# Optimization experiments

Measured on AMD Instinct MI355X. Metric: run time of the kernel, lower is better.

Reference implementation:

```python
import jax, jax.numpy as jnp
import numpy as np

NUM_HEADS = 16


def setup_inputs() -> dict:
    key = jax.random.key(0)
    ks = jax.random.split(key, 5)
    B, S, D = 2, 2048, 1024
    x = jax.random.normal(ks[0], (B, S, D), dtype=jnp.float32)
    # torch Linear weights are [out_features, in_features]; y = x @ W.T + b
    Wq = jax.random.normal(ks[1], (D, D), dtype=jnp.float32) * (D ** -0.5)
    Wk = jax.random.normal(ks[2], (D, D), dtype=jnp.float32) * (D ** -0.5)
    Wv = jax.random.normal(ks[3], (D, D), dtype=jnp.float32) * (D ** -0.5)
    Wo = jax.random.normal(ks[4], (D, D), dtype=jnp.float32) * (D ** -0.5)
    bo = jnp.zeros((D,), dtype=jnp.float32)
    return {"x": x, "Wq": Wq, "Wk": Wk, "Wv": Wv, "Wo": Wo, "bo": bo}


def reference(x, Wq, Wk, Wv, Wo, bo):
    B, S, D = x.shape
    H = NUM_HEADS
    dh = D // H
    # projections (torch Linear: x @ W.T)
    q = (x @ Wq.T).reshape(B, S, H, dh).transpose(0, 2, 1, 3)  # [B,H,S,dh]
    k = (x @ Wk.T).reshape(B, S, H, dh).transpose(0, 2, 1, 3)
    v = (x @ Wv.T).reshape(B, S, H, dh).transpose(0, 2, 1, 3)
    # NOTE: original code takes shape[-1] of the TRANSPOSED key (n,H,dh,S),
    # so the softmax scale is seq_length**-0.5 (a bug we reproduce faithfully).
    scale = jnp.asarray(S, x.dtype) ** -0.5
    scores = jnp.einsum("bhqd,bhkd->bhqk", q, k)  # [B,H,S,S]
    causal = jnp.triu(jnp.ones((S, S), dtype=bool), k=1)
    scores = jnp.where(causal, -jnp.inf, scores * scale)
    weights = jax.nn.softmax(scores, axis=-1)
    # dropout p=0.0 -> identity
    ctx = jnp.einsum("bhqk,bhkd->bhqd", weights, v)  # [B,H,S,dh]
    ctx = ctx.transpose(0, 2, 1, 3).reshape(B, S, D)
    return ctx @ Wo.T + bo
```

## Files before the change

kernel.cpp:

```cpp
#include <hip/hip_runtime.h>
#include <hip/hip_bf16.h>

#define B_SZ    2
#define S_LEN   2048
#define D_MODEL 1024
#define H_NUM   16
#define DH      64
#define M_TOT   (B_SZ * S_LEN)

#define QSCALE (0.022097086912079608f * 1.4426950408889634f)

typedef __attribute__((ext_vector_type(8)))  short          bf16x8;
typedef __attribute__((ext_vector_type(4)))  float          f32x4;
typedef __attribute__((ext_vector_type(16))) float          f32x16;
typedef __attribute__((ext_vector_type(8)))  unsigned short u16x8;
typedef __attribute__((ext_vector_type(4)))  unsigned short u16x4;

__device__ inline unsigned short f2bf(float f) {
  unsigned int u = __float_as_uint(f);
  u += 0x7fffu + ((u >> 16) & 1u);
  return (unsigned short)(u >> 16);
}

__device__ inline float bf2f(unsigned short u) {
  return __uint_as_float(((unsigned)u) << 16);
}

__device__ inline float fexp2(float x) {
#if __has_builtin(__builtin_amdgcn_exp2f)
  return __builtin_amdgcn_exp2f(x);
#else
  return exp2f(x);
#endif
}

__device__ inline unsigned cvt_pk_bf16(float lo, float hi) {
  unsigned r;
  asm("v_cvt_pk_bf16_f32 %0, %1, %2" : "=v"(r) : "v"(lo), "v"(hi));
  return r;
}

__device__ inline void gload16(const void* g, void* l) {
  __builtin_amdgcn_global_load_lds(
      (const __attribute__((address_space(1))) void*)g,
      (__attribute__((address_space(3))) void*)l, 16, 0, 0);
}

__global__ __launch_bounds__(256) void to_bf16_all(
    const float* __restrict__ x, const float* __restrict__ wq,
    const float* __restrict__ wk, const float* __restrict__ wv,
    const float* __restrict__ wo, unsigned short* __restrict__ xb,
    unsigned short* __restrict__ wqb, unsigned short* __restrict__ wkb,
    unsigned short* __restrict__ wvb, unsigned short* __restrict__ wob) {
  const size_t i = ((size_t)blockIdx.x * 256 + threadIdx.x) * 8;
  const float* src;
  unsigned short* dst;
  size_t off;
  if (i < 4194304)      { src = x;  dst = xb;  off = i; }
  else if (i < 5242880) { src = wq; dst = wqb; off = i - 4194304; }
  else if (i < 6291456) { src = wk; dst = wkb; off = i - 5242880; }
  else if (i < 7340032) { src = wv; dst = wvb; off = i - 6291456; }
  else                  { src = wo; dst = wob; off = i - 7340032; }
  f32x4 a = *(const f32x4*)(src + off);
  f32x4 b = *(const f32x4*)(src + off + 4);
  u16x8 o;
#pragma unroll
  for (int j = 0; j < 4; j++) { o[j] = f2bf(a[j]); o[4 + j] = f2bf(b[j]); }
  *(u16x8*)(dst + off) = o;
}

__device__ __forceinline__ void gemm_core(const unsigned short* __restrict__ A,
                                          const unsigned short* __restrict__ W,
                                          unsigned short (*Al)[128][32],
                                          unsigned short (*Bl)[128][32],
                                          int mbase, int nbase,
                                          f32x4 acc[4][4]) {
  const int tid  = threadIdx.x;
  const int lane = tid & 63;
  const int wid  = tid >> 6;
  const int wr   = wid >> 1, wc = wid & 1;
  const int g    = lane >> 4, lr = lane & 15;

  const int r0 = tid >> 2;
  const int cg = (tid & 3) ^ ((tid >> 3) & 3);

  const unsigned short* Abase = A + (size_t)(mbase + r0) * D_MODEL + cg * 8;
  const unsigned short* Wbase = W + (size_t)(nbase + r0) * D_MODEL + cg * 8;
  char* ldsA0 = (char*)Al + wid * 1024;
  char* ldsB0 = (char*)Bl + wid * 1024;

  gload16(Abase, ldsA0);
  gload16(Abase + (size_t)64 * D_MODEL, ldsA0 + 4096);
  gload16(Wbase, ldsB0);
  gload16(Wbase + (size_t)64 * D_MODEL, ldsB0 + 4096);

  const int NKT = D_MODEL / 32;
  for (int kt = 0; kt < NKT; ++kt) {
    const int cur = kt & 1;
    if (kt + 1 < NKT) {
      const unsigned short* As = Abase + (kt + 1) * 32;
      const unsigned short* Ws = Wbase + (kt + 1) * 32;
      char* la = ldsA0 + (cur ^ 1) * 8192;
      char* lb = ldsB0 + (cur ^ 1) * 8192;
      gload16(As, la);
      gload16(As + (size_t)64 * D_MODEL, la + 4096);
      gload16(Ws, lb);
      gload16(Ws + (size_t)64 * D_MODEL, lb + 4096);
      asm volatile("s_waitcnt vmcnt(4)" ::: "memory");
    } else {
      asm volatile("s_waitcnt vmcnt(0)" ::: "memory");
    }
    __builtin_amdgcn_s_barrier();

    bf16x8 af[4], bfr[4];
#pragma unroll
    for (int i = 0; i < 4; i++) {
      const int ra = wr * 64 + i * 16 + lr;
      af[i] = *(const bf16x8*)&Al[cur][ra][(g ^ ((ra >> 1) & 3)) * 8];
      const int rb = wc * 64 + i * 16 + lr;
      bfr[i] = *(const bf16x8*)&Bl[cur][rb][(g ^ ((rb >> 1) & 3)) * 8];
    }
    __builtin_amdgcn_s_setprio(1);
#pragma unroll
    for (int i = 0; i < 4; i++)
#pragma unroll
      for (int j = 0; j < 4; j++)
        acc[i][j] = __builtin_amdgcn_mfma_f32_16x16x32_bf16(af[i], bfr[j],
                                                            acc[i][j], 0, 0, 0);
    __builtin_amdgcn_s_setprio(0);
    asm volatile("" ::: "memory");
    __builtin_amdgcn_s_barrier();
  }
}

__global__ __launch_bounds__(256) void gemm_qkv(
    const unsigned short* __restrict__ xb, const unsigned short* __restrict__ wqb,
    const unsigned short* __restrict__ wkb, const unsigned short* __restrict__ wvb,
    unsigned short* __restrict__ qb, unsigned short* __restrict__ kb,
    unsigned short* __restrict__ vt) {
  __shared__ unsigned short Al[2][128][32];
  __shared__ unsigned short Bl[2][128][32];
  const int z = blockIdx.z;
  const unsigned short* W = (z == 0) ? wqb : (z == 1) ? wkb : wvb;
  unsigned short* dst = (z == 0) ? qb : (z == 1) ? kb : vt;
  const float sc = (z == 0) ? QSCALE : 1.0f;

  f32x4 acc[4][4];
#pragma unroll
  for (int i = 0; i < 4; i++)
#pragma unroll
    for (int j = 0; j < 4; j++) acc[i][j] = (f32x4){0.f, 0.f, 0.f, 0.f};

  const int mbase = blockIdx.y * 128, nbase = blockIdx.x * 128;
  gemm_core(xb, W, Al, Bl, mbase, nbase, acc);

  const int lane = threadIdx.x & 63, wid = threadIdx.x >> 6;
  const int wr = wid >> 1, wc = wid & 1, g = lane >> 4, lr = lane & 15;
#pragma unroll
  for (int i = 0; i < 4; i++) {
#pragma unroll
    for (int j = 0; j < 4; j++) {
      const int mg0 = mbase + wr * 64 + i * 16 + g * 4;
      const int ng  = nbase + wc * 64 + j * 16 + lr;
      if (z < 2) {
#pragma unroll
        for (int r = 0; r < 4; r++)
          dst[(size_t)(mg0 + r) * D_MODEL + ng] = f2bf(acc[i][j][r] * sc);
      } else {
        const int hh = ng >> 6, dd = ng & 63;
        const int bb = mg0 >> 11, ss = mg0 & 2047;
        u16x4 pk;
#pragma unroll
        for (int r = 0; r < 4; r++) pk[r] = f2bf(acc[i][j][r]);
        *(u16x4*)&dst[((size_t)((bb * H_NUM + hh) * DH + dd)) * S_LEN + ss] = pk;
      }
    }
  }
}

__global__ __launch_bounds__(256) void gemm_out(
    const unsigned short* __restrict__ cx, const unsigned short* __restrict__ wob,
    float* __restrict__ out, const float* __restrict__ bo) {
  __shared__ unsigned short Al[2][128][32];
  __shared__ unsigned short Bl[2][128][32];
  f32x4 acc[4][4];
#pragma unroll
  for (int i = 0; i < 4; i++)
#pragma unroll
    for (int j = 0; j < 4; j++) acc[i][j] = (f32x4){0.f, 0.f, 0.f, 0.f};

  const int mbase = blockIdx.y * 128, nbase = blockIdx.x * 128;
  gemm_core(cx, wob, Al, Bl, mbase, nbase, acc);

  const int lane = threadIdx.x & 63, wid = threadIdx.x >> 6;
  const int wr = wid >> 1, wc = wid & 1, g = lane >> 4, lr = lane & 15;
#pragma unroll
  for (int i = 0; i < 4; i++) {
#pragma unroll
    for (int j = 0; j < 4; j++) {
      const int mg0 = mbase + wr * 64 + i * 16 + g * 4;
      const int ng  = nbase + wc * 64 + j * 16 + lr;
      const float bv = bo[ng];
#pragma unroll
      for (int r = 0; r < 4; r++)
        out[(size_t)(mg0 + r) * D_MODEL + ng] = acc[i][j][r] + bv;
    }
  }
}

__device__ const unsigned att_sched[24] = {
    15u | (0u << 8)  | (16u << 16) | (0u << 24),
    15u | (16u << 8) | (32u << 16) | (1u << 24),
    7u  | (0u << 8)  | (16u << 16) | (2u << 24),
    14u | (0u << 8)  | (15u << 16) | (0u << 24),
    14u | (15u << 8) | (30u << 16) | (1u << 24),
    13u | (0u << 8)  | (14u << 16) | (0u << 24),
    13u | (14u << 8) | (28u << 16) | (1u << 24),
    6u  | (0u << 8)  | (14u << 16) | (2u << 24),
    12u | (0u << 8)  | (13u << 16) | (0u << 24),
    12u | (13u << 8) | (26u << 16) | (1u << 24),
    11u | (0u << 8)  | (12u << 16) | (0u << 24),
    11u | (12u << 8) | (24u << 16) | (1u << 24),
    5u  | (0u << 8)  | (12u << 16) | (2u << 24),
    10u | (0u << 8)  | (11u << 16) | (0u << 24),
    10u | (11u << 8) | (22u << 16) | (1u << 24),
    9u  | (0u << 8)  | (10u << 16) | (0u << 24),
    9u  | (10u << 8) | (20u << 16) | (1u << 24),
    4u  | (0u << 8)  | (10u << 16) | (2u << 24),
    8u  | (0u << 8)  | (9u << 16)  | (0u << 24),
    8u  | (9u << 8)  | (18u << 16) | (1u << 24),
    3u  | (0u << 8)  | (8u << 16)  | (2u << 24),
    2u  | (0u << 8)  | (6u << 16)  | (2u << 24),
    1u  | (0u << 8)  | (4u << 16)  | (2u << 24),
    0u  | (0u << 8)  | (2u << 16)  | (2u << 24),
};

__global__ __launch_bounds__(256) void attn_v5(
    const unsigned short* __restrict__ qb, const unsigned short* __restrict__ kb,
    const unsigned short* __restrict__ vt, unsigned short* __restrict__ cx,
    unsigned short* __restrict__ Opart, float* __restrict__ ml) {
  __shared__ alignas(16) char smem[32768];

  const int tid  = threadIdx.x;
  const int lane = tid & 63;
  const int w    = tid >> 6;
  const int hi   = lane >> 5;
  const int lq   = lane & 31;
  const int bid  = blockIdx.x;

  const unsigned ent = att_sched[bid >> 5];
  const int qi   = ent & 255;
  const int kt0  = (ent >> 8) & 255;
  const int kt1  = (ent >> 16) & 255;
  const int part = (ent >> 24) & 255;
  const int bh   = bid & 31;
  const int b    = bh >> 4, h = bh & 15;

  const int qg0  = qi * 128 + w * 32;
  const int tok0 = b * S_LEN + qg0;

  const int sr  = tid >> 3;
  const int scg = (tid & 7) ^ (sr & 7);
  const unsigned short* kbase =
      kb + (size_t)(b * S_LEN) * D_MODEL + h * DH + scg * 8;
  const unsigned short* vrow =
      vt + ((size_t)((b * H_NUM + h) * DH + sr)) * S_LEN + scg * 8;
  char* ldsK0 = smem + w * 1024;
  char* ldsV0 = smem + 16384 + w * 1024;

  bf16x8 qf[4];
  {
    const unsigned short* qrow =
        qb + (size_t)(tok0 + lq) * D_MODEL + h * DH + hi * 8;
#pragma unroll
    for (int ks = 0; ks < 4; ks++) qf[ks] = *(const bf16x8*)(qrow + ks * 16);
  }

  f32x16 ctx0, ctx1;
#pragma unroll
  for (int r = 0; r < 16; r++) { ctx0[r] = 0.f; ctx1[r] = 0.f; }
  float m_run = -1e30f, l_run = 0.f;

  const int ndiag = 2 * qi;

  {
    const unsigned short* sK = kbase + (size_t)(kt0 * 64 + sr) * D_MODEL;
    gload16(sK, ldsK0);
    gload16(sK + (size_t)32 * D_MODEL, ldsK0 + 4096);
    const unsigned short* sV = vrow + kt0 * 64;
    gload16(sV, ldsV0);
    gload16(sV + (size_t)32 * S_LEN, ldsV0 + 4096);
  }

  int ti = 0;
  for (int kt = kt0; kt < kt1; ++kt, ++ti) {
    const int cur = ti & 1;
    if (kt + 1 < kt1) {
      const int nb = cur ^ 1;
      const unsigned short* sK = kbase + (size_t)((kt + 1) * 64 + sr) * D_MODEL;
      gload16(sK, ldsK0 + nb * 8192);
      gload16(sK + (size_t)32 * D_MODEL, ldsK0 + nb * 8192 + 4096);
      const unsigned short* sV = vrow + (kt + 1) * 64;
      gload16(sV, ldsV0 + nb * 8192);
      gload16(sV + (size_t)32 * S_LEN, ldsV0 + nb * 8192 + 4096);
      asm volatile("s_waitcnt vmcnt(4)" ::: "memory");
    } else {
      asm volatile("s_waitcnt vmcnt(0)" ::: "memory");
    }
    __builtin_amdgcn_s_barrier();

    const char* Kc = smem + cur * 8192;
    const char* Vc = smem + 16384 + cur * 8192;

    f32x16 s0, s1;
#pragma unroll
    for (int r = 0; r < 16; r++) { s0[r] = 0.f; s1[r] = 0.f; }
    __builtin_amdgcn_s_setprio(1);
#pragma unroll
    for (int ks = 0; ks < 4; ks++) {
      const int c = ((ks * 2 + hi) ^ (lq & 7)) * 16;
      bf16x8 k0 = *(const bf16x8*)(Kc + lq * 128 + c);
      bf16x8 k1 = *(const bf16x8*)(Kc + (32 + lq) * 128 + c);
      s0 = __builtin_amdgcn_mfma_f32_32x32x16_bf16(k0, qf[ks], s0, 0, 0, 0);
      s1 = __builtin_amdgcn_mfma_f32_32x32x16_bf16(k1, qf[ks], s1, 0, 0, 0);
    }
    __builtin_amdgcn_s_setprio(0);

    if (kt >= ndiag) {
      const int relq = qg0 + lq - kt * 64 - 4 * hi;
#pragma unroll
      for (int r = 0; r < 16; r++) {
        const int ko = (r & 3) + 8 * (r >> 2);
        s0[r] = (ko > relq) ? -1e30f : s0[r];
        s1[r] = (ko + 32 > relq) ? -1e30f : s1[r];
      }
    }

    float tm[8];
#pragma unroll
    for (int j = 0; j < 8; j++)
      tm[j] = fmaxf(fmaxf(s0[j], s0[j + 8]), fmaxf(s1[j], s1[j + 8]));
#pragma unroll
    for (int j = 0; j < 4; j++) tm[j] = fmaxf(tm[j], tm[j + 4]);
    float pmax = fmaxf(fmaxf(tm[0], tm[2]), fmaxf(tm[1], tm[3]));
    pmax = fmaxf(pmax, __shfl_xor(pmax, 32));

    if (__any(pmax > m_run + 8.0f)) {
      const float mnew = fmaxf(m_run, pmax);
      const float al   = fexp2(m_run - mnew);
      m_run = mnew;
      l_run *= al;
#pragma unroll
      for (int r = 0; r < 16; r++) { ctx0[r] *= al; ctx1[r] *= al; }
    }

    float lsAcc[4];
#pragma unroll
    for (int ks = 0; ks < 4; ks++) {
      float p[8];
#pragma unroll
      for (int j = 0; j < 8; j++) {
        const int r = (ks & 1) * 8 + j;
        const float sv = (ks < 2) ? s0[r] : s1[r];
        p[j] = fexp2(sv - m_run);
      }
      lsAcc[ks] = ((p[0] + p[1]) + (p[2] + p[3])) +
                  ((p[4] + p[5]) + (p[6] + p[7]));
      const unsigned w01 = cvt_pk_bf16(p[0], p[1]);
      const unsigned w23 = cvt_pk_bf16(p[2], p[3]);
      const unsigned w45 = cvt_pk_bf16(p[4], p[5]);
      const unsigned w67 = cvt_pk_bf16(p[6], p[7]);
      const unsigned x01 = __shfl_xor(w01, 32);
      const unsigned x23 = __shfl_xor(w23, 32);
      const unsigned x45 = __shfl_xor(w45, 32);
      const unsigned x67 = __shfl_xor(w67, 32);
      union { unsigned u[4]; bf16x8 v; } pw;
      pw.u[0] = hi ? x45 : w01;
      pw.u[1] = hi ? x67 : w23;
      pw.u[2] = hi ? w45 : x01;
      pw.u[3] = hi ? w67 : x23;
      const int c = ((ks * 2 + hi) ^ (lq & 7)) * 16;
      bf16x8 v0 = *(const bf16x8*)(Vc + lq * 128 + c);
      bf16x8 v1 = *(const bf16x8*)(Vc + (32 + lq) * 128 + c);
      __builtin_amdgcn_s_setprio(1);
      ctx0 = __builtin_amdgcn_mfma_f32_32x32x16_bf16(v0, pw.v, ctx0, 0, 0, 0);
      ctx1 = __builtin_amdgcn_mfma_f32_32x32x16_bf16(v1, pw.v, ctx1, 0, 0, 0);
      __builtin_amdgcn_s_setprio(0);
    }
    l_run += (lsAcc[0] + lsAcc[1]) + (lsAcc[2] + lsAcc[3]);
    asm volatile("" ::: "memory");
    __builtin_amdgcn_s_barrier();
  }

  unsigned short (*Tl)[32][72] = (unsigned short (*)[32][72])smem;
  const float lfull = l_run + __shfl_xor(l_run, 32);
  const float inv   = (part == 2) ? (1.0f / lfull) : 1.0f;
#pragma unroll
  for (int rp = 0; rp < 8; rp++) {
    const int r  = rp * 2;
    const int d0 = (r & 3) + 8 * (r >> 2) + 4 * hi;
    *(unsigned*)&Tl[w][lq][d0] = cvt_pk_bf16(ctx0[r] * inv, ctx0[r + 1] * inv);
    *(unsigned*)&Tl[w][lq][32 + d0] =
        cvt_pk_bf16(ctx1[r] * inv, ctx1[r + 1] * inv);
  }
  asm volatile("s_waitcnt lgkmcnt(0)" ::: "memory");
  const int q2 = lane >> 1;
  if (part == 2) {
#pragma unroll
    for (int i = 0; i < 4; i++) {
      const int ch = (lane & 1) * 4 + i;
      u16x8 vv = *(const u16x8*)&Tl[w][q2][ch * 8];
      *(u16x8*)&cx[(size_t)(tok0 + q2) * D_MODEL + h * DH + ch * 8] = vv;
    }
  } else {
    const int pidx = (qi - 8) * 2 + part;
    unsigned short* od =
        Opart + ((size_t)(pidx * 32 + bh) * 128 + w * 32 + q2) * 64;
#pragma unroll
    for (int i = 0; i < 4; i++) {
      const int ch = (lane & 1) * 4 + i;
      u16x8 vv = *(const u16x8*)&Tl[w][q2][ch * 8];
      *(u16x8*)&od[ch * 8] = vv;
    }
    if (hi == 0) {
      float2 v2 = make_float2(m_run, lfull);
      *(float2*)&ml[((size_t)(pidx * 32 + bh) * 128 + w * 32 + lq) * 2] = v2;
    }
  }
}

__global__ __launch_bounds__(256) void attn_combine(
    const unsigned short* __restrict__ Opart, const float* __restrict__ ml,
    unsigned short* __restrict__ cx) {
  const int gid    = blockIdx.x * 256 + threadIdx.x;
  const int sub    = gid & 7;
  const int row_id = gid >> 3;
  const int row    = row_id & 127;
  const int bh     = (row_id >> 7) & 31;
  const int qi8    = row_id >> 12;
  const int pA = qi8 * 2, pB = qi8 * 2 + 1;

  const size_t ra = (size_t)(pA * 32 + bh) * 128 + row;
  const size_t rb = (size_t)(pB * 32 + bh) * 128 + row;
  const float mA = ml[ra * 2], lA = ml[ra * 2 + 1];
  const float mB = ml[rb * 2], lB = ml[rb * 2 + 1];
  const float m  = fmaxf(mA, mB);
  const float wA = fexp2(mA - m), wB = fexp2(mB - m);
  const float inv = 1.0f / (lA * wA + lB * wB);

  u16x8 a = *(const u16x8*)&Opart[ra * 64 + sub * 8];
  u16x8 c = *(const u16x8*)&Opart[rb * 64 + sub * 8];
  u16x8 o;
#pragma unroll
  for (int j = 0; j < 8; j++)
    o[j] = f2bf((bf2f(a[j]) * wA + bf2f(c[j]) * wB) * inv);

  const int b = bh >> 4, h = bh & 15;
  const int tok = b * S_LEN + (qi8 + 8) * 128 + row;
  *(u16x8*)&cx[(size_t)tok * D_MODEL + h * DH + sub * 8] = o;
}

extern "C" void kernel_launch(void* const* d_in, const int* in_sizes, int n_in,
                              void* d_out, int out_size, void* d_ws,
                              size_t ws_size, hipStream_t stream) {
  const float* x  = (const float*)d_in[0];
  const float* Wq = (const float*)d_in[1];
  const float* Wk = (const float*)d_in[2];
  const float* Wv = (const float*)d_in[3];
  const float* Wo = (const float*)d_in[4];
  const float* bo = (const float*)d_in[5];
  float* out = (float*)d_out;

  unsigned short* xb  = (unsigned short*)d_ws;
  unsigned short* wqb = xb  + (size_t)M_TOT * D_MODEL;
  unsigned short* wkb = wqb + (size_t)D_MODEL * D_MODEL;
  unsigned short* wvb = wkb + (size_t)D_MODEL * D_MODEL;
  unsigned short* wob = wvb + (size_t)D_MODEL * D_MODEL;
  unsigned short* qb  = wob + (size_t)D_MODEL * D_MODEL;
  unsigned short* kb  = qb  + (size_t)M_TOT * D_MODEL;
  unsigned short* vt  = kb  + (size_t)M_TOT * D_MODEL;
  unsigned short* cx  = vt  + (size_t)M_TOT * D_MODEL;
  unsigned short* Opart = xb;
  float*          ml    = (float*)wqb;

  to_bf16_all<<<4096, 256, 0, stream>>>(x, Wq, Wk, Wv, Wo, xb, wqb, wkb, wvb,
                                        wob);
  gemm_qkv<<<dim3(D_MODEL / 128, M_TOT / 128, 3), 256, 0, stream>>>(
      xb, wqb, wkb, wvb, qb, kb, vt);
  attn_v5<<<dim3(768), 256, 0, stream>>>(qb, kb, vt, cx, Opart, ml);
  attn_combine<<<dim3(1024), 256, 0, stream>>>(Opart, ml, cx);
  gemm_out<<<dim3(D_MODEL / 128, M_TOT / 128), 256, 0, stream>>>(cx, wob, out,
                                                                 bo);
}
```

Before: 123.2 us.

## Split causal attention into finer KV chunks with generalized multi-part combine

Replaces the 24-entry attention schedule (one split into two KV halves plus paired short tiles) with a 40-entry schedule. Each query tile is now cut into 1-4 KV chunks of roughly 5-8 tiles, giving 1280 blocks with more even work. The combine kernel is generalized to merge up to four partials, reusing the cx buffer for part 0. The shuffle-plus-select P exchange is replaced with v_permlane32_swap, and launch bounds now request 5 blocks per CU. This gains load balance and occupancy at the cost of more partial-result traffic and a larger combine pass.

Result: slower. 160.3 us (+30.1%).

```diff
diff --git a/kernel.cpp b/kernel.cpp
--- a/kernel.cpp
+++ b/kernel.cpp
@@ -208,34 +208,32 @@
   }
 }
 
-__device__ const unsigned att_sched[24] = {
-    15u | (0u << 8)  | (16u << 16) | (0u << 24),
-    15u | (16u << 8) | (32u << 16) | (1u << 24),
-    7u  | (0u << 8)  | (16u << 16) | (2u << 24),
-    14u | (0u << 8)  | (15u << 16) | (0u << 24),
-    14u | (15u << 8) | (30u << 16) | (1u << 24),
-    13u | (0u << 8)  | (14u << 16) | (0u << 24),
-    13u | (14u << 8) | (28u << 16) | (1u << 24),
-    6u  | (0u << 8)  | (14u << 16) | (2u << 24),
-    12u | (0u << 8)  | (13u << 16) | (0u << 24),
-    12u | (13u << 8) | (26u << 16) | (1u << 24),
-    11u | (0u << 8)  | (12u << 16) | (0u << 24),
-    11u | (12u << 8) | (24u << 16) | (1u << 24),
-    5u  | (0u << 8)  | (12u << 16) | (2u << 24),
-    10u | (0u << 8)  | (11u << 16) | (0u << 24),
-    10u | (11u << 8) | (22u << 16) | (1u << 24),
-    9u  | (0u << 8)  | (10u << 16) | (0u << 24),
-    9u  | (10u << 8) | (20u << 16) | (1u << 24),
-    4u  | (0u << 8)  | (10u << 16) | (2u << 24),
-    8u  | (0u << 8)  | (9u << 16)  | (0u << 24),
-    8u  | (9u << 8)  | (18u << 16) | (1u << 24),
-    3u  | (0u << 8)  | (8u << 16)  | (2u << 24),
-    2u  | (0u << 8)  | (6u << 16)  | (2u << 24),
-    1u  | (0u << 8)  | (4u << 16)  | (2u << 24),
-    0u  | (0u << 8)  | (2u << 16)  | (2u << 24),
+#define ENT(qi, k0, k1, p) ((unsigned)(qi) | ((unsigned)(k0) << 8) | \
+                            ((unsigned)(k1) << 16) | ((unsigned)(p) << 24))
+__device__ const unsigned att_sched[40] = {
+    ENT(3, 0, 8, 0),   ENT(7, 0, 8, 0),   ENT(7, 8, 16, 1),
+    ENT(10, 0, 8, 0),  ENT(11, 0, 8, 0),  ENT(11, 8, 16, 1),
+    ENT(11, 16, 24, 2),ENT(14, 0, 8, 0),  ENT(14, 15, 23, 2),
+    ENT(15, 0, 8, 0),  ENT(15, 8, 16, 1), ENT(15, 16, 24, 2),
+    ENT(15, 24, 32, 3),
+    ENT(6, 0, 7, 0),   ENT(6, 7, 14, 1),  ENT(9, 0, 7, 0),
+    ENT(9, 7, 14, 1),  ENT(10, 8, 15, 1), ENT(10, 15, 22, 2),
+    ENT(12, 0, 7, 0),  ENT(12, 13, 20, 2),ENT(13, 0, 7, 0),
+    ENT(13, 7, 14, 1), ENT(13, 14, 21, 2),ENT(13, 21, 28, 3),
+    ENT(14, 8, 15, 1), ENT(14, 23, 30, 3),
+    ENT(2, 0, 6, 0),   ENT(5, 0, 6, 0),   ENT(5, 6, 12, 1),
+    ENT(8, 0, 6, 0),   ENT(8, 6, 12, 1),  ENT(8, 12, 18, 2),
+    ENT(9, 14, 20, 2), ENT(12, 7, 13, 1), ENT(12, 20, 26, 3),
+    ENT(4, 0, 5, 0),   ENT(4, 5, 10, 1),  ENT(1, 0, 4, 0),
+    ENT(0, 0, 2, 0),
 };
-
-__global__ __launch_bounds__(256) void attn_v5(
+__device__ const int att_chunks[16]   = {1,1,1,1, 2,2,2,2, 3,3,3,3, 4,4,4,4};
+__device__ const int att_mlbase[16]   = {0,1,2,3, 4,6,8,10, 12,15,18,21,
+                                         24,28,32,36};
+__device__ const int att_opbase[16]   = {0,0,0,0, 0,1,2,3, 4,6,8,10,
+                                         12,15,18,21};
+
+__global__ __launch_bounds__(256, 5) void attn_v6(
     const unsigned short* __restrict__ qb, const unsigned short* __restrict__ kb,
     const unsigned short* __restrict__ vt, unsigned short* __restrict__ cx,
     unsigned short* __restrict__ Opart, float* __restrict__ ml) {
@@ -253,6 +251,7 @@
   const int kt0  = (ent >> 8) & 255;
   const int kt1  = (ent >> 16) & 255;
   const int part = (ent >> 24) & 255;
+  const int nch  = att_chunks[qi];
   const int bh   = bid & 31;
   const int b    = bh >> 4, h = bh & 15;
 
@@ -366,19 +365,17 @@
       }
       lsAcc[ks] = ((p[0] + p[1]) + (p[2] + p[3])) +
                   ((p[4] + p[5]) + (p[6] + p[7]));
-      const unsigned w01 = cvt_pk_bf16(p[0], p[1]);
-      const unsigned w23 = cvt_pk_bf16(p[2], p[3]);
-      const unsigned w45 = cvt_pk_bf16(p[4], p[5]);
-      const unsigned w67 = cvt_pk_bf16(p[6], p[7]);
-      const unsigned x01 = __shfl_xor(w01, 32);
-      const unsigned x23 = __shfl_xor(w23, 32);
-      const unsigned x45 = __shfl_xor(w45, 32);
-      const unsigned x67 = __shfl_xor(w67, 32);
+      unsigned a0 = cvt_pk_bf16(p[0], p[1]);
+      unsigned a1 = cvt_pk_bf16(p[4], p[5]);
+      unsigned b0 = cvt_pk_bf16(p[2], p[3]);
+      unsigned b1 = cvt_pk_bf16(p[6], p[7]);
+      asm("v_permlane32_swap_b32 %0, %1" : "+v"(a0), "+v"(a1));
+      asm("v_permlane32_swap_b32 %0, %1" : "+v"(b0), "+v"(b1));
       union { unsigned u[4]; bf16x8 v; } pw;
-      pw.u[0] = hi ? x45 : w01;
-      pw.u[1] = hi ? x67 : w23;
-      pw.u[2] = hi ? w45 : x01;
-      pw.u[3] = hi ? w67 : x23;
+      pw.u[0] = a0;
+      pw.u[1] = b0;
+      pw.u[2] = a1;
+      pw.u[3] = b1;
       const int c = ((ks * 2 + hi) ^ (lq & 7)) * 16;
       bf16x8 v0 = *(const bf16x8*)(Vc + lq * 128 + c);
       bf16x8 v1 = *(const bf16x8*)(Vc + (32 + lq) * 128 + c);
@@ -394,7 +391,7 @@
 
   unsigned short (*Tl)[32][72] = (unsigned short (*)[32][72])smem;
   const float lfull = l_run + __shfl_xor(l_run, 32);
-  const float inv   = (part == 2) ? (1.0f / lfull) : 1.0f;
+  const float inv   = (nch == 1) ? (1.0f / lfull) : 1.0f;
 #pragma unroll
   for (int rp = 0; rp < 8; rp++) {
     const int r  = rp * 2;
@@ -405,58 +402,80 @@
   }
   asm volatile("s_waitcnt lgkmcnt(0)" ::: "memory");
   const int q2 = lane >> 1;
-  if (part == 2) {
-#pragma unroll
-    for (int i = 0; i < 4; i++) {
-      const int ch = (lane & 1) * 4 + i;
-      u16x8 vv = *(const u16x8*)&Tl[w][q2][ch * 8];
-      *(u16x8*)&cx[(size_t)(tok0 + q2) * D_MODEL + h * DH + ch * 8] = vv;
-    }
+  unsigned short* dstp;
+  if (nch == 1 || part == 0) {
+    dstp = &cx[(size_t)(tok0 + q2) * D_MODEL + h * DH];
   } else {
-    const int pidx = (qi - 8) * 2 + part;
-    unsigned short* od =
-        Opart + ((size_t)(pidx * 32 + bh) * 128 + w * 32 + q2) * 64;
-#pragma unroll
-    for (int i = 0; i < 4; i++) {
-      const int ch = (lane & 1) * 4 + i;
-      u16x8 vv = *(const u16x8*)&Tl[w][q2][ch * 8];
-      *(u16x8*)&od[ch * 8] = vv;
-    }
-    if (hi == 0) {
-      float2 v2 = make_float2(m_run, lfull);
-      *(float2*)&ml[((size_t)(pidx * 32 + bh) * 128 + w * 32 + lq) * 2] = v2;
-    }
+    dstp = Opart + ((size_t)((att_opbase[qi] + part - 1) * 32 + bh) * 128 +
+                    w * 32 + q2) * 64;
+  }
+#pragma unroll
+  for (int i = 0; i < 4; i++) {
+    const int ch = (lane & 1) * 4 + i;
+    u16x8 vv = *(const u16x8*)&Tl[w][q2][ch * 8];
+    *(u16x8*)&dstp[ch * 8] = vv;
+  }
+  if (nch > 1 && hi == 0) {
+    float2 v2 = make_float2(m_run, lfull);
+    *(float2*)&ml[((size_t)((att_mlbase[qi] + part) * 32 + bh) * 128 +
+                   w * 32 + lq) * 2] = v2;
   }
 }
 
 __global__ __launch_bounds__(256) void attn_combine(
     const unsigned short* __restrict__ Opart, const float* __restrict__ ml,
     unsigned short* __restrict__ cx) {
-  const int gid    = blockIdx.x * 256 + threadIdx.x;
-  const int sub    = gid & 7;
-  const int row_id = gid >> 3;
-  const int row    = row_id & 127;
-  const int bh     = (row_id >> 7) & 31;
-  const int qi8    = row_id >> 12;
-  const int pA = qi8 * 2, pB = qi8 * 2 + 1;
-
-  const size_t ra = (size_t)(pA * 32 + bh) * 128 + row;
-  const size_t rb = (size_t)(pB * 32 + bh) * 128 + row;
-  const float mA = ml[ra * 2], lA = ml[ra * 2 + 1];
-  const float mB = ml[rb * 2], lB = ml[rb * 2 + 1];
-  const float m  = fmaxf(mA, mB);
-  const float wA = fexp2(mA - m), wB = fexp2(mB - m);
-  const float inv = 1.0f / (lA * wA + lB * wB);
-
-  u16x8 a = *(const u16x8*)&Opart[ra * 64 + sub * 8];
-  u16x8 c = *(const u16x8*)&Opart[rb * 64 + sub * 8];
+  const int gid = blockIdx.x * 256 + threadIdx.x;
+  const int sub = gid & 7;
+  const int row = (gid >> 3) & 127;
+  const int bh  = (gid >> 10) & 31;
+  const int qi  = 4 + (gid >> 15);
+  const int nch = att_chunks[qi];
+  const int b = bh >> 4, h = bh & 15;
+  const int tok = b * S_LEN + qi * 128 + row;
+
+  float mv[4], lv[4];
+  float m = -1e30f;
+#pragma unroll 4
+  for (int p = 0; p < 4; p++) {
+    if (p < nch) {
+      const size_t mi =
+          ((size_t)((att_mlbase[qi] + p) * 32 + bh) * 128 + row) * 2;
+      mv[p] = ml[mi];
+      lv[p] = ml[mi + 1];
+      m = fmaxf(m, mv[p]);
+    }
+  }
+  float denom = 0.f;
+  float wgt[4];
+#pragma unroll 4
+  for (int p = 0; p < 4; p++) {
+    if (p < nch) {
+      wgt[p] = fexp2(mv[p] - m);
+      denom += lv[p] * wgt[p];
+    }
+  }
+  const float inv = 1.0f / denom;
+
+  float acc[8];
+  {
+    u16x8 a = *(const u16x8*)&cx[(size_t)tok * D_MODEL + h * DH + sub * 8];
+#pragma unroll
+    for (int j = 0; j < 8; j++) acc[j] = bf2f(a[j]) * wgt[0];
+  }
+#pragma unroll 4
+  for (int p = 1; p < 4; p++) {
+    if (p < nch) {
+      const unsigned short* src =
+          Opart + ((size_t)((att_opbase[qi] + p - 1) * 32 + bh) * 128 + row) * 64;
+      u16x8 a = *(const u16x8*)&src[sub * 8];
+#pragma unroll
+      for (int j = 0; j < 8; j++) acc[j] += bf2f(a[j]) * wgt[p];
+    }
+  }
   u16x8 o;
 #pragma unroll
-  for (int j = 0; j < 8; j++)
-    o[j] = f2bf((bf2f(a[j]) * wA + bf2f(c[j]) * wB) * inv);
-
-  const int b = bh >> 4, h = bh & 15;
-  const int tok = b * S_LEN + (qi8 + 8) * 128 + row;
+  for (int j = 0; j < 8; j++) o[j] = f2bf(acc[j] * inv);
   *(u16x8*)&cx[(size_t)tok * D_MODEL + h * DH + sub * 8] = o;
 }
 
@@ -481,14 +500,14 @@
   unsigned short* vt  = kb  + (size_t)M_TOT * D_MODEL;
   unsigned short* cx  = vt  + (size_t)M_TOT * D_MODEL;
   unsigned short* Opart = xb;
-  float*          ml    = (float*)wqb;
+  float*          ml    = (float*)(xb + (size_t)768 * 8192);
 
   to_bf16_all<<<4096, 256, 0, stream>>>(x, Wq, Wk, Wv, Wo, xb, wqb, wkb, wvb,
                                         wob);
   gemm_qkv<<<dim3(D_MODEL / 128, M_TOT / 128, 3), 256, 0, stream>>>(
       xb, wqb, wkb, wvb, qb, kb, vt);
-  attn_v5<<<dim3(768), 256, 0, stream>>>(qb, kb, vt, cx, Opart, ml);
-  attn_combine<<<dim3(1024), 256, 0, stream>>>(Opart, ml, cx);
+  attn_v6<<<dim3(1280), 256, 0, stream>>>(qb, kb, vt, cx, Opart, ml);
+  attn_combine<<<dim3(1536), 256, 0, stream>>>(Opart, ml, cx);
   gemm_out<<<dim3(D_MODEL / 128, M_TOT / 128), 256, 0, stream>>>(cx, wob, out,
                                                                  bo);
 }
```
